# Kernel optimization log

Measured on AMD Instinct MI355X. Metric: run time of the kernel, lower is better.

The kernel has to match this reference:

```python
import jax, jax.numpy as jnp
import numpy as np

N_NODES = 200000
N_EDGES = 6400000
D_IN, D_HID, D_OUT = 128, 16, 172


def gcn_conv(x, edge_index, W, b, n):
    """PyG GCNConv: add self-loops, symmetric D^-1/2 A D^-1/2 normalization,
    linear projection, scatter-add aggregation, bias."""
    src, dst = edge_index[0], edge_index[1]
    loops = jnp.arange(n, dtype=edge_index.dtype)
    src = jnp.concatenate([src, loops])
    dst = jnp.concatenate([dst, loops])
    # in-degree with self-loops (>= 1, so rsqrt is safe)
    deg = jax.ops.segment_sum(jnp.ones_like(dst, dtype=x.dtype), dst, num_segments=n)
    dinv = jax.lax.rsqrt(deg)
    lin = x @ W  # [n, d_out]
    norm = dinv[src] * dinv[dst]  # per-edge normalization
    msg = lin[src] * norm[:, None]  # gather + scale
    out = jax.ops.segment_sum(msg, dst, num_segments=n)  # scatter-add
    return out + b


def setup_inputs() -> dict:
    key = jax.random.key(0)
    k1, k2, k3, k4, k5, k6 = jax.random.split(key, 6)
    x = jax.random.normal(k1, (N_NODES, D_IN), dtype=jnp.float32)
    edge_index = jax.random.randint(k2, (2, N_EDGES), 0, N_NODES, dtype=jnp.int64)
    W1 = jax.random.normal(k3, (D_IN, D_HID), dtype=jnp.float32) * (1.0 / np.sqrt(D_IN))
    b1 = jnp.zeros((D_HID,), dtype=jnp.float32)
    W2 = jax.random.normal(k4, (D_HID, D_OUT), dtype=jnp.float32) * (1.0 / np.sqrt(D_HID))
    b2 = jnp.zeros((D_OUT,), dtype=jnp.float32)
    return {"x": x, "edge_index": edge_index, "W1": W1, "b1": b1, "W2": W2, "b2": b2}


def reference(x, edge_index, W1, b1, W2, b2):
    n = x.shape[0]
    # CRD: GCNConv -> relu (dropout is identity in eval mode)
    h = jax.nn.relu(gcn_conv(x, edge_index, W1, b1, n))
    # CLS: GCNConv -> log_softmax over classes
    logits = gcn_conv(h, edge_index, W2, b2, n)
    return jax.nn.log_softmax(logits, axis=1)
```

## Files before the change

### kernel.cpp

```cpp
#include <hip/hip_runtime.h>
#include <hip/hip_fp16.h>

#define N_NODES 200000
#define N_EDGES 6400000
#define D_IN    128
#define D_HID   16
#define D_OUT   172

#define NS1     800
#define EPB     8000
#define SBN     782
#define SB_NODES 256

#define O_BTOT  0
#define O_BASE  1024
#define O_CNT1  2048
#define O_COL   2048
#define O_ROW   6402048
#define O_DINV  6602112
#define O_PACK  6802112
#define O_F16A  6802112
#define O_F16B  8402112
#define O_AGG2  10002112

__global__ __launch_bounds__(256) void k_hist1(const int* __restrict__ dst,
                                               unsigned* __restrict__ counts) {
    __shared__ unsigned cnt[SBN];
    for (int i = threadIdx.x; i < SBN; i += 256) cnt[i] = 0;
    __syncthreads();
    const int* dp = dst + blockIdx.x * EPB;
    for (int i = threadIdx.x; i < EPB; i += 256)
        atomicAdd(&cnt[dp[i] >> 8], 1u);
    __syncthreads();
    unsigned* out = counts + (size_t)blockIdx.x * SBN;
    for (int i = threadIdx.x; i < SBN; i += 256) out[i] = cnt[i];
}

__global__ __launch_bounds__(256) void k_scan_col(unsigned* __restrict__ counts,
                                                  unsigned* __restrict__ btot) {
    __shared__ unsigned arr[NS1];
    int b = blockIdx.x;
    for (int i = threadIdx.x; i < NS1; i += 256)
        arr[i] = counts[(size_t)i * SBN + b];
    __syncthreads();
    if (threadIdx.x < 64) {
        int l = threadIdx.x;
        int lo = l * 13, hi = min(lo + 13, NS1);
        unsigned sum = 0;
        for (int i = lo; i < hi; ++i) sum += arr[i];
        unsigned incl = sum;
#pragma unroll
        for (int o = 1; o < 64; o <<= 1) {
            unsigned tmp = __shfl_up(incl, o);
            if (l >= o) incl += tmp;
        }
        if (l == 63) btot[b] = incl;
        unsigned run = incl - sum;
        for (int i = lo; i < hi; ++i) { unsigned v = arr[i]; arr[i] = run; run += v; }
    }
    __syncthreads();
    for (int i = threadIdx.x; i < NS1; i += 256)
        counts[(size_t)i * SBN + b] = arr[i];
}

__global__ __launch_bounds__(64) void k_scan_base(const unsigned* __restrict__ btot,
                                                  unsigned* __restrict__ base) {
    int l = threadIdx.x;
    int lo = l * 13, hi = min(lo + 13, SBN);
    unsigned sum = 0;
    for (int i = lo; i < hi; ++i) sum += btot[i];
    unsigned incl = sum;
#pragma unroll
    for (int o = 1; o < 64; o <<= 1) {
        unsigned tmp = __shfl_up(incl, o);
        if (l >= o) incl += tmp;
    }
    unsigned run = incl - sum;
    for (int i = lo; i < hi; ++i) { unsigned v = btot[i]; base[i] = run; run += v; }
    if (l == 63) base[SBN] = incl;
}

__global__ __launch_bounds__(256) void k_scatter1(const int* __restrict__ src,
                                                  const int* __restrict__ dst,
                                                  const unsigned* __restrict__ counts,
                                                  const unsigned* __restrict__ base,
                                                  unsigned* __restrict__ packed) {
    __shared__ unsigned       sdat[EPB];
    __shared__ unsigned short sbkt[EPB];
    __shared__ unsigned cnt[SBN];
    __shared__ unsigned off[SBN];
    __shared__ unsigned gbs[SBN];
    __shared__ unsigned wsum[4];
    int t = threadIdx.x;
    const unsigned* crow = counts + (size_t)blockIdx.x * SBN;
    for (int i = t; i < SBN; i += 256) { cnt[i] = 0; gbs[i] = base[i] + crow[i]; }
    __syncthreads();
    const int* sp = src + blockIdx.x * EPB;
    const int* dp = dst + blockIdx.x * EPB;
    for (int i = t; i < EPB; i += 256) atomicAdd(&cnt[dp[i] >> 8], 1u);
    __syncthreads();
    int lane = t & 63, wid = t >> 6;
    int b0 = t * 4;
    unsigned c0v = (b0 + 0 < SBN) ? cnt[b0 + 0] : 0;
    unsigned c1v = (b0 + 1 < SBN) ? cnt[b0 + 1] : 0;
    unsigned c2v = (b0 + 2 < SBN) ? cnt[b0 + 2] : 0;
    unsigned c3v = (b0 + 3 < SBN) ? cnt[b0 + 3] : 0;
    unsigned mysum = c0v + c1v + c2v + c3v;
    unsigned incl = mysum;
#pragma unroll
    for (int o = 1; o < 64; o <<= 1) {
        unsigned tmp = __shfl_up(incl, o);
        if (lane >= o) incl += tmp;
    }
    if (lane == 63) wsum[wid] = incl;
    __syncthreads();
    unsigned wbase = 0;
    for (int w = 0; w < wid; ++w) wbase += wsum[w];
    unsigned run = wbase + incl - mysum;
    if (b0 + 0 < SBN) { off[b0 + 0] = run; run += c0v; }
    if (b0 + 1 < SBN) { off[b0 + 1] = run; run += c1v; }
    if (b0 + 2 < SBN) { off[b0 + 2] = run; run += c2v; }
    if (b0 + 3 < SBN) { off[b0 + 3] = run; run += c3v; }
    __syncthreads();
    for (int i = t; i < EPB; i += 256) {
        int s = sp[i], d = dp[i];
        unsigned b = (unsigned)d >> 8;
        unsigned slot = atomicAdd(&off[b], 1u);
        sdat[slot] = ((unsigned)(d & (SB_NODES - 1)) << 18) | (unsigned)s;
        sbkt[slot] = (unsigned short)b;
    }
    __syncthreads();
    for (int i = t; i < EPB; i += 256) {
        unsigned b = sbkt[i];
        unsigned start = off[b] - cnt[b];
        packed[gbs[b] + (i - start)] = sdat[i];
    }
}

__global__ __launch_bounds__(256) void k_csr(const unsigned* __restrict__ packed,
                                             const unsigned* __restrict__ base,
                                             int* __restrict__ rowptr,
                                             float* __restrict__ dinv,
                                             int* __restrict__ col) {
    __shared__ unsigned cnt[SB_NODES];
    __shared__ unsigned off[SB_NODES];
    __shared__ unsigned wsum[4];
    int t = threadIdx.x, sb = blockIdx.x;
    unsigned beg = base[sb], end = base[sb + 1];
    cnt[t] = 0;
    __syncthreads();
    for (unsigned i = beg + t; i < end; i += 256)
        atomicAdd(&cnt[packed[i] >> 18], 1u);
    __syncthreads();
    unsigned e = cnt[t];
    int lane = t & 63, wid = t >> 6;
    unsigned incl = e;
#pragma unroll
    for (int o = 1; o < 64; o <<= 1) {
        unsigned tmp = __shfl_up(incl, o);
        if (lane >= o) incl += tmp;
    }
    if (lane == 63) wsum[wid] = incl;
    __syncthreads();
    unsigned wbase = 0;
    for (int w = 0; w < wid; ++w) wbase += wsum[w];
    unsigned ex = wbase + incl - e;
    off[t] = ex;
    int n0 = sb * SB_NODES + t;
    if (n0 <= N_NODES) rowptr[n0] = (int)(beg + ex);
    if (n0 <  N_NODES) dinv[n0]   = rsqrtf((float)(e + 1));
    __syncthreads();
    for (unsigned i = beg + t; i < end; i += 256) {
        unsigned p = packed[i];
        unsigned slot = atomicAdd(&off[p >> 18], 1u);
        col[beg + slot] = (int)(p & 0x3FFFFu);
    }
}

__global__ __launch_bounds__(256) void k_lin1(const float* __restrict__ x,
                                              const float* __restrict__ W1,
                                              const float* __restrict__ dinv,
                                              __half* __restrict__ lin) {
    __shared__ float sW[D_IN * D_HID];
    for (int t = threadIdx.x; t < D_IN * D_HID; t += 256) sW[t] = W1[t];
    __syncthreads();

    int g  = threadIdx.x & 3;
    int nl = threadIdx.x >> 2;
    int n  = blockIdx.x * 64 + nl;

    float acc[16];
#pragma unroll
    for (int j = 0; j < 16; ++j) acc[j] = 0.f;

    const float4* xr = (const float4*)(x + (size_t)n * D_IN + g * 32);
#pragma unroll
    for (int i = 0; i < 8; ++i) {
        float4 xv = xr[i];
        int k = g * 32 + i * 4;
#pragma unroll
        for (int j = 0; j < 16; ++j) {
            acc[j] += xv.x * sW[(k + 0) * 16 + j] + xv.y * sW[(k + 1) * 16 + j]
                    + xv.z * sW[(k + 2) * 16 + j] + xv.w * sW[(k + 3) * 16 + j];
        }
    }
#pragma unroll
    for (int j = 0; j < 16; ++j) {
        acc[j] += __shfl_xor(acc[j], 1);
        acc[j] += __shfl_xor(acc[j], 2);
    }
    float di = dinv[n];
    ushort4 pk;
    pk.x = __half_as_ushort(__float2half(acc[g * 4 + 0] * di));
    pk.y = __half_as_ushort(__float2half(acc[g * 4 + 1] * di));
    pk.z = __half_as_ushort(__float2half(acc[g * 4 + 2] * di));
    pk.w = __half_as_ushort(__float2half(acc[g * 4 + 3] * di));
    *(ushort4*)(lin + (size_t)n * 16 + g * 4) = pk;
}

template <int MODE>
__global__ __launch_bounds__(256) void k_gather(const int* __restrict__ rowptr,
                                                const int* __restrict__ col,
                                                const float* __restrict__ dinv,
                                                const __half2* __restrict__ fin,
                                                const float* __restrict__ bias,
                                                void* __restrict__ outv) {
    int t = threadIdx.x;
    int n = blockIdx.x * 32 + (t >> 3);
    int lane = t & 7;
    int beg = rowptr[n], end = rowptr[n + 1];
    float2 a0 = __half22float2(fin[n * 8 + lane]);
    float2 a1 = {0,0}, a2 = {0,0}, a3 = {0,0};
    float2 a4 = {0,0}, a5 = {0,0}, a6 = {0,0}, a7 = {0,0};
    int i = beg;
    for (; i + 8 <= end; i += 8) {
        int s0 = col[i + 0], s1 = col[i + 1], s2 = col[i + 2], s3 = col[i + 3];
        int s4 = col[i + 4], s5 = col[i + 5], s6 = col[i + 6], s7 = col[i + 7];
        __half2 h0 = fin[s0 * 8 + lane], h1 = fin[s1 * 8 + lane];
        __half2 h2 = fin[s2 * 8 + lane], h3 = fin[s3 * 8 + lane];
        __half2 h4 = fin[s4 * 8 + lane], h5 = fin[s5 * 8 + lane];
        __half2 h6 = fin[s6 * 8 + lane], h7 = fin[s7 * 8 + lane];
        float2 f0 = __half22float2(h0), f1 = __half22float2(h1);
        float2 f2 = __half22float2(h2), f3 = __half22float2(h3);
        float2 f4 = __half22float2(h4), f5 = __half22float2(h5);
        float2 f6 = __half22float2(h6), f7 = __half22float2(h7);
        a0.x += f0.x; a0.y += f0.y;  a1.x += f1.x; a1.y += f1.y;
        a2.x += f2.x; a2.y += f2.y;  a3.x += f3.x; a3.y += f3.y;
        a4.x += f4.x; a4.y += f4.y;  a5.x += f5.x; a5.y += f5.y;
        a6.x += f6.x; a6.y += f6.y;  a7.x += f7.x; a7.y += f7.y;
    }
    for (; i < end; ++i) {
        float2 f = __half22float2(fin[col[i] * 8 + lane]);
        a0.x += f.x; a0.y += f.y;
    }
    float vx = ((a0.x + a1.x) + (a2.x + a3.x)) + ((a4.x + a5.x) + (a6.x + a7.x));
    float vy = ((a0.y + a1.y) + (a2.y + a3.y)) + ((a4.y + a5.y) + (a6.y + a7.y));
    float dd = dinv[n];
    vx *= dd; vy *= dd;
    if (MODE) {
        float2 b2v = ((const float2*)bias)[lane];
        vx = fmaxf(vx + b2v.x, 0.f) * dd;
        vy = fmaxf(vy + b2v.y, 0.f) * dd;
        ((__half2*)outv)[n * 8 + lane] = __floats2half2_rn(vx, vy);
    } else {
        ((float2*)outv)[n * 8 + lane] = make_float2(vx, vy);
    }
}

#define SLP 173
__global__ __launch_bounds__(256) void k_out(const float* __restrict__ agg2,
                                             const float* __restrict__ W2,
                                             const float* __restrict__ b2,
                                             float* __restrict__ out) {
    __shared__ float sl[64 * SLP];
    __shared__ float pm[4][64];
    __shared__ float ps[4][64];
    __shared__ float sls[64];
    int t   = threadIdx.x;
    int wid = __builtin_amdgcn_readfirstlane(t >> 6);
    int nl  = t & 63;
    int n   = blockIdx.x * 64 + nl;

    const float4* ar = (const float4*)(agg2 + (size_t)n * 16);
    float4 a0 = ar[0], a1 = ar[1], a2 = ar[2], a3 = ar[3];
    float a[16] = {a0.x, a0.y, a0.z, a0.w, a1.x, a1.y, a1.z, a1.w,
                   a2.x, a2.y, a2.z, a2.w, a3.x, a3.y, a3.z, a3.w};

    float m = -INFINITY, s = 0.f;
    float* srow = sl + nl * SLP;
    for (int i = 0; i < 43; ++i) {
        int c = wid + 4 * i;
        float l = b2[c];
#pragma unroll
        for (int k = 0; k < 16; ++k) l += a[k] * W2[k * D_OUT + c];
        srow[c] = l;
        if (l > m) { s *= __expf(m - l); m = l; }
        s += __expf(l - m);
    }
    pm[wid][nl] = m; ps[wid][nl] = s;
    __syncthreads();
    if (wid == 0) {
        float m0 = pm[0][nl], m1 = pm[1][nl], m2 = pm[2][nl], m3 = pm[3][nl];
        float M  = fmaxf(fmaxf(m0, m1), fmaxf(m2, m3));
        float S  = ps[0][nl] * __expf(m0 - M) + ps[1][nl] * __expf(m1 - M)
                 + ps[2][nl] * __expf(m2 - M) + ps[3][nl] * __expf(m3 - M);
        sls[nl] = M + __logf(S);
    }
    __syncthreads();
    float* ob = out + (size_t)blockIdx.x * 64 * D_OUT;
    for (int idx = t; idx < 64 * D_OUT; idx += 256) {
        int node = idx / D_OUT, c = idx - node * D_OUT;
        ob[idx] = sl[node * SLP + c] - sls[node];
    }
}

extern "C" void kernel_launch(void* const* d_in, const int* in_sizes, int n_in,
                              void* d_out, int out_size, void* d_ws, size_t ws_size,
                              hipStream_t stream) {
    const float* x     = (const float*)d_in[0];
    const int*   edges = (const int*)d_in[1];
    const float* W1    = (const float*)d_in[2];
    const float* b1    = (const float*)d_in[3];
    const float* W2    = (const float*)d_in[4];
    const float* b2    = (const float*)d_in[5];
    float*       out   = (float*)d_out;

    const int* src = edges;
    const int* dst = edges + N_EDGES;

    unsigned* ws     = (unsigned*)d_ws;
    unsigned* btot   = ws + O_BTOT;
    unsigned* base   = ws + O_BASE;
    unsigned* counts = ws + O_CNT1;
    int*      col    = (int*)(ws + O_COL);
    int*      rowptr = (int*)(ws + O_ROW);
    float*    dinv   = (float*)(ws + O_DINV);
    unsigned* packed = ws + O_PACK;
    __half*   f16a   = (__half*)(ws + O_F16A);
    __half*   f16b   = (__half*)(ws + O_F16B);
    float*    agg2   = (float*)(ws + O_AGG2);

    k_hist1    <<<NS1, 256, 0, stream>>>(dst, counts);
    k_scan_col <<<SBN, 256, 0, stream>>>(counts, btot);
    k_scan_base<<<1,    64, 0, stream>>>(btot, base);
    k_scatter1 <<<NS1, 256, 0, stream>>>(src, dst, counts, base, packed);
    k_csr      <<<SBN, 256, 0, stream>>>(packed, base, rowptr, dinv, col);

    k_lin1     <<<N_NODES / 64, 256, 0, stream>>>(x, W1, dinv, f16a);
    k_gather<1><<<N_NODES / 32, 256, 0, stream>>>(rowptr, col, dinv,
                                                  (const __half2*)f16a, b1, f16b);

    k_gather<0><<<N_NODES / 32, 256, 0, stream>>>(rowptr, col, dinv,
                                                  (const __half2*)f16b, b1, agg2);
    k_out      <<<N_NODES / 64, 256, 0, stream>>>(agg2, W2, b2, out);
}
```

Baseline: 429.2 us.

## Reuse histogram counts in scatter, widen gather loads, store fp16 logits in k_out

The column scan now writes its prefix sums to a separate buffer, so k_scatter1 reads the per-block bucket counts instead of re-histogramming its edges with shared atomics. The gather kernels now have 4 lanes per node each loading 8 bytes (four halves), so one block covers 64 nodes instead of 32. k_out keeps logits in fp16 shared memory and computes the softmax in two passes (max first, then sum of exponentials), which removes the per-element rescale exponentials. The fp16 logit staging loses precision in the output, and the new scan buffer starts at an offset that overlaps the col region, which assumes col is written only later.

Result: faster. 397.3 us (-7.4%).

```diff
diff --git a/kernel.cpp b/kernel.cpp
--- a/kernel.cpp
+++ b/kernel.cpp
@@ -15,6 +15,7 @@
 #define O_BTOT  0
 #define O_BASE  1024
 #define O_CNT1  2048
+#define O_SCN   627648
 #define O_COL   2048
 #define O_ROW   6402048
 #define O_DINV  6602112
@@ -36,7 +37,8 @@
     for (int i = threadIdx.x; i < SBN; i += 256) out[i] = cnt[i];
 }
 
-__global__ __launch_bounds__(256) void k_scan_col(unsigned* __restrict__ counts,
+__global__ __launch_bounds__(256) void k_scan_col(const unsigned* __restrict__ counts,
+                                                  unsigned* __restrict__ scn,
                                                   unsigned* __restrict__ btot) {
     __shared__ unsigned arr[NS1];
     int b = blockIdx.x;
@@ -60,7 +62,7 @@
     }
     __syncthreads();
     for (int i = threadIdx.x; i < NS1; i += 256)
-        counts[(size_t)i * SBN + b] = arr[i];
+        scn[(size_t)i * SBN + b] = arr[i];
 }
 
 __global__ __launch_bounds__(64) void k_scan_base(const unsigned* __restrict__ btot,
@@ -83,6 +85,7 @@
 __global__ __launch_bounds__(256) void k_scatter1(const int* __restrict__ src,
                                                   const int* __restrict__ dst,
                                                   const unsigned* __restrict__ counts,
+                                                  const unsigned* __restrict__ scn,
                                                   const unsigned* __restrict__ base,
                                                   unsigned* __restrict__ packed) {
     __shared__ unsigned       sdat[EPB];
@@ -93,11 +96,11 @@
     __shared__ unsigned wsum[4];
     int t = threadIdx.x;
     const unsigned* crow = counts + (size_t)blockIdx.x * SBN;
-    for (int i = t; i < SBN; i += 256) { cnt[i] = 0; gbs[i] = base[i] + crow[i]; }
-    __syncthreads();
-    const int* sp = src + blockIdx.x * EPB;
-    const int* dp = dst + blockIdx.x * EPB;
-    for (int i = t; i < EPB; i += 256) atomicAdd(&cnt[dp[i] >> 8], 1u);
+    const unsigned* srow = scn    + (size_t)blockIdx.x * SBN;
+    for (int i = t; i < SBN; i += 256) {
+        cnt[i] = crow[i];
+        gbs[i] = base[i] + srow[i];
+    }
     __syncthreads();
     int lane = t & 63, wid = t >> 6;
     int b0 = t * 4;
@@ -122,6 +125,8 @@
     if (b0 + 2 < SBN) { off[b0 + 2] = run; run += c2v; }
     if (b0 + 3 < SBN) { off[b0 + 3] = run; run += c3v; }
     __syncthreads();
+    const int* sp = src + blockIdx.x * EPB;
+    const int* dp = dst + blockIdx.x * EPB;
     for (int i = t; i < EPB; i += 256) {
         int s = sp[i], d = dp[i];
         unsigned b = (unsigned)d >> 8;
@@ -218,61 +223,84 @@
     *(ushort4*)(lin + (size_t)n * 16 + g * 4) = pk;
 }
 
+#define H2F2(u) __half22float2(*(const __half2*)&(u))
 template <int MODE>
 __global__ __launch_bounds__(256) void k_gather(const int* __restrict__ rowptr,
                                                 const int* __restrict__ col,
                                                 const float* __restrict__ dinv,
-                                                const __half2* __restrict__ fin,
+                                                const uint2* __restrict__ fin,
                                                 const float* __restrict__ bias,
                                                 void* __restrict__ outv) {
     int t = threadIdx.x;
-    int n = blockIdx.x * 32 + (t >> 3);
-    int lane = t & 7;
+    int n = blockIdx.x * 64 + (t >> 2);
+    int lane = t & 3;
     int beg = rowptr[n], end = rowptr[n + 1];
-    float2 a0 = __half22float2(fin[n * 8 + lane]);
-    float2 a1 = {0,0}, a2 = {0,0}, a3 = {0,0};
-    float2 a4 = {0,0}, a5 = {0,0}, a6 = {0,0}, a7 = {0,0};
+    uint2 su = fin[n * 4 + lane];
+    float2 sl0 = H2F2(su.x), sl1 = H2F2(su.y);
+    float ax0 = sl0.x, ay0 = sl0.y, az0 = sl1.x, aw0 = sl1.y;
+    float ax1 = 0, ay1 = 0, az1 = 0, aw1 = 0;
+    float ax2 = 0, ay2 = 0, az2 = 0, aw2 = 0;
+    float ax3 = 0, ay3 = 0, az3 = 0, aw3 = 0;
+    float ax4 = 0, ay4 = 0, az4 = 0, aw4 = 0;
+    float ax5 = 0, ay5 = 0, az5 = 0, aw5 = 0;
+    float ax6 = 0, ay6 = 0, az6 = 0, aw6 = 0;
+    float ax7 = 0, ay7 = 0, az7 = 0, aw7 = 0;
     int i = beg;
     for (; i + 8 <= end; i += 8) {
         int s0 = col[i + 0], s1 = col[i + 1], s2 = col[i + 2], s3 = col[i + 3];
         int s4 = col[i + 4], s5 = col[i + 5], s6 = col[i + 6], s7 = col[i + 7];
-        __half2 h0 = fin[s0 * 8 + lane], h1 = fin[s1 * 8 + lane];
-        __half2 h2 = fin[s2 * 8 + lane], h3 = fin[s3 * 8 + lane];
-        __half2 h4 = fin[s4 * 8 + lane], h5 = fin[s5 * 8 + lane];
-        __half2 h6 = fin[s6 * 8 + lane], h7 = fin[s7 * 8 + lane];
-        float2 f0 = __half22float2(h0), f1 = __half22float2(h1);
-        float2 f2 = __half22float2(h2), f3 = __half22float2(h3);
-        float2 f4 = __half22float2(h4), f5 = __half22float2(h5);
-        float2 f6 = __half22float2(h6), f7 = __half22float2(h7);
-        a0.x += f0.x; a0.y += f0.y;  a1.x += f1.x; a1.y += f1.y;
-        a2.x += f2.x; a2.y += f2.y;  a3.x += f3.x; a3.y += f3.y;
-        a4.x += f4.x; a4.y += f4.y;  a5.x += f5.x; a5.y += f5.y;
-        a6.x += f6.x; a6.y += f6.y;  a7.x += f7.x; a7.y += f7.y;
+        uint2 h0 = fin[s0 * 4 + lane], h1 = fin[s1 * 4 + lane];
+        uint2 h2 = fin[s2 * 4 + lane], h3 = fin[s3 * 4 + lane];
+        uint2 h4 = fin[s4 * 4 + lane], h5 = fin[s5 * 4 + lane];
+        uint2 h6 = fin[s6 * 4 + lane], h7 = fin[s7 * 4 + lane];
+        float2 l0 = H2F2(h0.x), m0 = H2F2(h0.y);
+        float2 l1 = H2F2(h1.x), m1 = H2F2(h1.y);
+        float2 l2 = H2F2(h2.x), m2 = H2F2(h2.y);
+        float2 l3 = H2F2(h3.x), m3 = H2F2(h3.y);
+        float2 l4 = H2F2(h4.x), m4 = H2F2(h4.y);
+        float2 l5 = H2F2(h5.x), m5 = H2F2(h5.y);
+        float2 l6 = H2F2(h6.x), m6 = H2F2(h6.y);
+        float2 l7 = H2F2(h7.x), m7 = H2F2(h7.y);
+        ax0 += l0.x; ay0 += l0.y; az0 += m0.x; aw0 += m0.y;
+        ax1 += l1.x; ay1 += l1.y; az1 += m1.x; aw1 += m1.y;
+        ax2 += l2.x; ay2 += l2.y; az2 += m2.x; aw2 += m2.y;
+        ax3 += l3.x; ay3 += l3.y; az3 += m3.x; aw3 += m3.y;
+        ax4 += l4.x; ay4 += l4.y; az4 += m4.x; aw4 += m4.y;
+        ax5 += l5.x; ay5 += l5.y; az5 += m5.x; aw5 += m5.y;
+        ax6 += l6.x; ay6 += l6.y; az6 += m6.x; aw6 += m6.y;
+        ax7 += l7.x; ay7 += l7.y; az7 += m7.x; aw7 += m7.y;
     }
     for (; i < end; ++i) {
-        float2 f = __half22float2(fin[col[i] * 8 + lane]);
-        a0.x += f.x; a0.y += f.y;
-    }
-    float vx = ((a0.x + a1.x) + (a2.x + a3.x)) + ((a4.x + a5.x) + (a6.x + a7.x));
-    float vy = ((a0.y + a1.y) + (a2.y + a3.y)) + ((a4.y + a5.y) + (a6.y + a7.y));
+        uint2 h = fin[col[i] * 4 + lane];
+        float2 l = H2F2(h.x), m = H2F2(h.y);
+        ax0 += l.x; ay0 += l.y; az0 += m.x; aw0 += m.y;
+    }
+    float vx = ((ax0 + ax1) + (ax2 + ax3)) + ((ax4 + ax5) + (ax6 + ax7));
+    float vy = ((ay0 + ay1) + (ay2 + ay3)) + ((ay4 + ay5) + (ay6 + ay7));
+    float vz = ((az0 + az1) + (az2 + az3)) + ((az4 + az5) + (az6 + az7));
+    float vw = ((aw0 + aw1) + (aw2 + aw3)) + ((aw4 + aw5) + (aw6 + aw7));
     float dd = dinv[n];
-    vx *= dd; vy *= dd;
+    vx *= dd; vy *= dd; vz *= dd; vw *= dd;
     if (MODE) {
-        float2 b2v = ((const float2*)bias)[lane];
-        vx = fmaxf(vx + b2v.x, 0.f) * dd;
-        vy = fmaxf(vy + b2v.y, 0.f) * dd;
-        ((__half2*)outv)[n * 8 + lane] = __floats2half2_rn(vx, vy);
+        float4 b4 = ((const float4*)bias)[lane];
+        vx = fmaxf(vx + b4.x, 0.f) * dd;
+        vy = fmaxf(vy + b4.y, 0.f) * dd;
+        vz = fmaxf(vz + b4.z, 0.f) * dd;
+        vw = fmaxf(vw + b4.w, 0.f) * dd;
+        __half2 o0 = __floats2half2_rn(vx, vy), o1 = __floats2half2_rn(vz, vw);
+        uint2 o; o.x = *(const unsigned*)&o0; o.y = *(const unsigned*)&o1;
+        ((uint2*)outv)[n * 4 + lane] = o;
     } else {
-        ((float2*)outv)[n * 8 + lane] = make_float2(vx, vy);
-    }
-}
-
-#define SLP 173
+        ((float4*)outv)[n * 4 + lane] = make_float4(vx, vy, vz, vw);
+    }
+}
+
+#define SLP 174
 __global__ __launch_bounds__(256) void k_out(const float* __restrict__ agg2,
                                              const float* __restrict__ W2,
                                              const float* __restrict__ b2,
                                              float* __restrict__ out) {
-    __shared__ float sl[64 * SLP];
+    __shared__ __half sl[64 * SLP];
     __shared__ float pm[4][64];
     __shared__ float ps[4][64];
     __shared__ float sls[64];
@@ -286,31 +314,31 @@
     float a[16] = {a0.x, a0.y, a0.z, a0.w, a1.x, a1.y, a1.z, a1.w,
                    a2.x, a2.y, a2.z, a2.w, a3.x, a3.y, a3.z, a3.w};
 
-    float m = -INFINITY, s = 0.f;
-    float* srow = sl + nl * SLP;
+    float m = -INFINITY;
+    __half* srow = sl + nl * SLP;
     for (int i = 0; i < 43; ++i) {
         int c = wid + 4 * i;
         float l = b2[c];
 #pragma unroll
         for (int k = 0; k < 16; ++k) l += a[k] * W2[k * D_OUT + c];
-        srow[c] = l;
-        if (l > m) { s *= __expf(m - l); m = l; }
-        s += __expf(l - m);
-    }
-    pm[wid][nl] = m; ps[wid][nl] = s;
-    __syncthreads();
-    if (wid == 0) {
-        float m0 = pm[0][nl], m1 = pm[1][nl], m2 = pm[2][nl], m3 = pm[3][nl];
-        float M  = fmaxf(fmaxf(m0, m1), fmaxf(m2, m3));
-        float S  = ps[0][nl] * __expf(m0 - M) + ps[1][nl] * __expf(m1 - M)
-                 + ps[2][nl] * __expf(m2 - M) + ps[3][nl] * __expf(m3 - M);
-        sls[nl] = M + __logf(S);
-    }
+        srow[c] = __float2half(l);
+        m = fmaxf(m, l);
+    }
+    pm[wid][nl] = m;
+    __syncthreads();
+    float M = fmaxf(fmaxf(pm[0][nl], pm[1][nl]), fmaxf(pm[2][nl], pm[3][nl]));
+    float s = 0.f;
+    for (int i = 0; i < 43; ++i)
+        s += __expf(__half2float(srow[wid + 4 * i]) - M);
+    ps[wid][nl] = s;
+    __syncthreads();
+    if (wid == 0)
+        sls[nl] = M + __logf(ps[0][nl] + ps[1][nl] + ps[2][nl] + ps[3][nl]);
     __syncthreads();
     float* ob = out + (size_t)blockIdx.x * 64 * D_OUT;
     for (int idx = t; idx < 64 * D_OUT; idx += 256) {
         int node = idx / D_OUT, c = idx - node * D_OUT;
-        ob[idx] = sl[node * SLP + c] - sls[node];
+        ob[idx] = __half2float(sl[node * SLP + c]) - sls[node];
     }
 }
 
@@ -332,6 +360,7 @@
     unsigned* btot   = ws + O_BTOT;
     unsigned* base   = ws + O_BASE;
     unsigned* counts = ws + O_CNT1;
+    unsigned* scn    = ws + O_SCN;
     int*      col    = (int*)(ws + O_COL);
     int*      rowptr = (int*)(ws + O_ROW);
     float*    dinv   = (float*)(ws + O_DINV);
@@ -341,16 +370,16 @@
     float*    agg2   = (float*)(ws + O_AGG2);
 
     k_hist1    <<<NS1, 256, 0, stream>>>(dst, counts);
-    k_scan_col <<<SBN, 256, 0, stream>>>(counts, btot);
+    k_scan_col <<<SBN, 256, 0, stream>>>(counts, scn, btot);
     k_scan_base<<<1,    64, 0, stream>>>(btot, base);
-    k_scatter1 <<<NS1, 256, 0, stream>>>(src, dst, counts, base, packed);
+    k_scatter1 <<<NS1, 256, 0, stream>>>(src, dst, counts, scn, base, packed);
     k_csr      <<<SBN, 256, 0, stream>>>(packed, base, rowptr, dinv, col);
 
     k_lin1     <<<N_NODES / 64, 256, 0, stream>>>(x, W1, dinv, f16a);
-    k_gather<1><<<N_NODES / 32, 256, 0, stream>>>(rowptr, col, dinv,
-                                                  (const __half2*)f16a, b1, f16b);
-
-    k_gather<0><<<N_NODES / 32, 256, 0, stream>>>(rowptr, col, dinv,
-                                                  (const __half2*)f16b, b1, agg2);
+    k_gather<1><<<N_NODES / 64, 256, 0, stream>>>(rowptr, col, dinv,
+                                                  (const uint2*)f16a, b1, f16b);
+
+    k_gather<0><<<N_NODES / 64, 256, 0, stream>>>(rowptr, col, dinv,
+                                                  (const uint2*)f16b, b1, agg2);
     k_out      <<<N_NODES / 64, 256, 0, stream>>>(agg2, W2, b2, out);
 }
```
